# Performance work log

Hardware: AMD Instinct MI355X
Metric: run time of the kernel (lower is better)

The kernel has to match this reference:

```python
import jax, jax.numpy as jnp
import numpy as np

B, T, D = 4, 2048, 2048
P, K, ALPHA, R = 512, 16, 4, 32
E_RATIO = 0.8
EPS = 1e-6


def rmsnorm(x, g):
    return x * jax.lax.rsqrt(jnp.mean(x * x, axis=-1, keepdims=True) + EPS) * g


def dale_signs():
    # first e_ratio*P neurons excitatory (+1), rest inhibitory (-1)
    return jnp.where(jnp.arange(P) < int(E_RATIO * P), 1.0, -1.0)


def quant_dale(w, signs):
    # STE sign-quantization with per-neuron mean-abs scale + Dale's-law sign constraint
    scale = jnp.mean(jnp.abs(w), axis=-1, keepdims=True)  # [P,1]
    q = scale * signs[:, None] * jnp.ones_like(w)         # magnitude=scale, sign fixed per neuron
    return w + jax.lax.stop_gradient(q - w)


def synapse_graph(x, idx, w):
    # x: [B,T,D], idx: [P,K] int, w: [P,K] -> dendritic inputs [B,T,P,K]
    return jnp.take(x, idx, axis=-1) * w


def perceptron(x_dend, Wp, Wout, signs):
    Wq = quant_dale(Wp, signs)                              # [P,K]
    u = jnp.einsum('btpk,pk->btp', x_dend, Wq)              # [B,T,P]
    f = jax.nn.sigmoid(u)                                   # gate [B,T,P]
    f_out = quant_dale(Wout, signs)                         # [P,ALPHA]
    y = (f * u)[..., None] * f_out                          # [B,T,P,ALPHA]
    return u, f, y, f_out


def low_rank_ssm(t, f, s0, U, V, Wgate, bgate):
    # t,f: [B,T,P]; s0: [B,R]. Low-rank gated linear scan in R dims.
    z = jnp.einsum('btp,pr->btr', t, U)
    lam = jax.nn.sigmoid(jnp.einsum('btp,pr->btr', f, Wgate) + bgate)

    def step(s, inp):
        z_t, l_t = inp
        s = l_t * s + z_t
        return s, s

    sT, S = jax.lax.scan(step, s0, (jnp.moveaxis(z, 1, 0), jnp.moveaxis(lam, 1, 0)))
    tilde = jnp.einsum('btr,rp->btp', jnp.moveaxis(S, 0, 1), V)
    return tilde, sT


def flatten_ports(y):
    return y.reshape(*y.shape[:-2], P * ALPHA)


def setup_inputs() -> dict:
    key = jax.random.key(0)
    ks = jax.random.split(key, 14)
    sc = 0.1
    return {
        'x': jax.random.normal(ks[0], (B, T, D), jnp.float32),
        'state': jnp.zeros((B, R), jnp.float32),
        'g1': jnp.ones((D,), jnp.float32),
        'g2': jnp.ones((D,), jnp.float32),
        'idx_ssm': jax.random.randint(ks[1], (P, K), 0, D),
        'wg_ssm': jax.random.normal(ks[2], (P, K), jnp.float32) * sc,
        'idx_mlp': jax.random.randint(ks[3], (P, K), 0, D),
        'wg_mlp': jax.random.normal(ks[4], (P, K), jnp.float32) * sc,
        'Wp_ssm': jax.random.normal(ks[5], (P, K), jnp.float32) * sc,
        'Wout_ssm': jax.random.normal(ks[6], (P, ALPHA), jnp.float32) * sc,
        'Wp_mlp': jax.random.normal(ks[7], (P, K), jnp.float32) * sc,
        'Wout_mlp': jax.random.normal(ks[8], (P, ALPHA), jnp.float32) * sc,
        'U': jax.random.normal(ks[9], (P, R), jnp.float32) * sc,
        'V': jax.random.normal(ks[10], (R, P), jnp.float32) * sc,
        'Wgate': jax.random.normal(ks[11], (P, R), jnp.float32) * sc,
        'bgate': jnp.zeros((R,), jnp.float32),
    }


def reference(x, state, g1, g2, idx_ssm, wg_ssm, idx_mlp, wg_mlp,
              Wp_ssm, Wout_ssm, Wp_mlp, Wout_mlp, U, V, Wgate, bgate):
    signs = dale_signs()
    # --- SSM branch ---
    h1 = rmsnorm(x, g1)
    x_dend_ssm = synapse_graph(h1, idx_ssm, wg_ssm)
    u_ssm, f_ssm, _, f_out = perceptron(x_dend_ssm, Wp_ssm, Wout_ssm, signs)
    t_ssm = f_ssm * u_ssm
    tilde_t, new_state = low_rank_ssm(t_ssm, f_ssm, state, U, V, Wgate, bgate)
    y_ssm = (f_ssm * tilde_t)[..., None] * f_out            # [B,T,P,ALPHA]
    x_after = x + flatten_ports(y_ssm)
    # --- MLP branch ---
    h2 = rmsnorm(x_after, g2)
    x_dend_mlp = synapse_graph(h2, idx_mlp, wg_mlp)
    _, _, y_mlp, _ = perceptron(x_dend_mlp, Wp_mlp, Wout_mlp, signs)
    x_out = x_after + flatten_ports(y_mlp)
    return x_out, new_state
```

## Files before the change

kernel.cpp:

```cpp
#include <hip/hip_runtime.h>
#include <hip/hip_bf16.h>

#define B_ 4
#define T_ 2048
#define D_ 2048
#define P_ 512
#define K_ 16
#define ALPHA_ 4
#define R_ 32
#define NE_ 409
#define EPS_ 1e-6f
#define G_ 4

typedef unsigned short u16;

__device__ __forceinline__ float sigmoidf_(float x) {
  return 1.0f / (1.0f + __expf(-x));
}
__device__ __forceinline__ float bfb2f(u16 u) {
  return __uint_as_float(((unsigned int)u) << 16);
}
__device__ __forceinline__ u16 f2bfb(float f) {
  __hip_bfloat16 h = __float2bfloat16(f);
  return *reinterpret_cast<u16*>(&h);
}

__global__ void k_scalars(const float* __restrict__ Wp_s, const float* __restrict__ Wo_s,
                          const float* __restrict__ Wp_m, const float* __restrict__ Wo_m,
                          float* __restrict__ wq_s, float* __restrict__ fo_s,
                          float* __restrict__ wq_m, float* __restrict__ fo_m) {
  int p = blockIdx.x * blockDim.x + threadIdx.x;
  if (p >= P_) return;
  float sgn = (p < NE_) ? 1.0f : -1.0f;
  float a = 0, b = 0, c = 0, d = 0;
#pragma unroll
  for (int k = 0; k < K_; k++) {
    a += fabsf(Wp_s[p * K_ + k]);
    c += fabsf(Wp_m[p * K_ + k]);
  }
#pragma unroll
  for (int k = 0; k < ALPHA_; k++) {
    b += fabsf(Wo_s[p * ALPHA_ + k]);
    d += fabsf(Wo_m[p * ALPHA_ + k]);
  }
  wq_s[p] = sgn * a * (1.0f / K_);
  fo_s[p] = sgn * b * (1.0f / ALPHA_);
  wq_m[p] = sgn * c * (1.0f / K_);
  fo_m[p] = sgn * d * (1.0f / ALPHA_);
}

__global__ __launch_bounds__(256) void k_phase1(
    const float* __restrict__ x, const float* __restrict__ g1,
    const int* __restrict__ idx, const float* __restrict__ wg,
    const float* __restrict__ U, const float* __restrict__ Wgt,
    const float* __restrict__ bg, const float* __restrict__ wq,
    float* __restrict__ f_ssm, float* __restrict__ z, float* __restrict__ lam) {
  __shared__ u16 h1[G_][D_];
  __shared__ float fl[G_][P_];
  __shared__ float tl[G_][P_];
  __shared__ float red[G_][4];
  __shared__ float zp[G_][R_][4];
  __shared__ float lp[G_][R_][4];

  int tid = threadIdx.x;
  int token0 = blockIdx.x * G_;
  int b = token0 >> 11;
  int t0 = token0 & (T_ - 1);

  float gv[8];
  {
    const float4* gp = reinterpret_cast<const float4*>(g1 + tid * 8);
    *reinterpret_cast<float4*>(&gv[0]) = gp[0];
    *reinterpret_cast<float4*>(&gv[4]) = gp[1];
  }
  float xv[G_][8];
  float ssv[G_];
#pragma unroll
  for (int tok = 0; tok < G_; tok++) {
    const float4* xp = reinterpret_cast<const float4*>(x + (size_t)(token0 + tok) * D_ + tid * 8);
    *reinterpret_cast<float4*>(&xv[tok][0]) = xp[0];
    *reinterpret_cast<float4*>(&xv[tok][4]) = xp[1];
    float ss = 0;
#pragma unroll
    for (int i = 0; i < 8; i++) ss += xv[tok][i] * xv[tok][i];
    ssv[tok] = ss;
  }
#pragma unroll
  for (int tok = 0; tok < G_; tok++) {
    float s = ssv[tok];
#pragma unroll
    for (int off = 32; off; off >>= 1) s += __shfl_down(s, off);
    if ((tid & 63) == 0) red[tok][tid >> 6] = s;
  }
  __syncthreads();
#pragma unroll
  for (int tok = 0; tok < G_; tok++) {
    float inv = rsqrtf((red[tok][0] + red[tok][1] + red[tok][2] + red[tok][3]) * (1.0f / D_) + EPS_);
    u16 tmp[8];
#pragma unroll
    for (int i = 0; i < 8; i++) tmp[i] = f2bfb(xv[tok][i] * inv * gv[i]);
    *reinterpret_cast<uint4*>(&h1[tok][tid * 8]) = *reinterpret_cast<const uint4*>(tmp);
  }
  __syncthreads();

#pragma unroll
  for (int j = 0; j < 2; j++) {
    int p = tid + j * 256;
    union { int4 v[4]; int s[16]; } iu;
    const int4* ip = reinterpret_cast<const int4*>(idx + p * K_);
    iu.v[0] = ip[0]; iu.v[1] = ip[1]; iu.v[2] = ip[2]; iu.v[3] = ip[3];
    union { float4 v[4]; float s[16]; } wu;
    const float4* wp = reinterpret_cast<const float4*>(wg + p * K_);
    wu.v[0] = wp[0]; wu.v[1] = wp[1]; wu.v[2] = wp[2]; wu.v[3] = wp[3];
    float wqp = wq[p];
#pragma unroll
    for (int tok = 0; tok < G_; tok++) {
      float acc = 0;
#pragma unroll
      for (int k = 0; k < K_; k++) acc += bfb2f(h1[tok][iu.s[k]]) * wu.s[k];
      float u = wqp * acc;
      float f = sigmoidf_(u);
      fl[tok][p] = f;
      tl[tok][p] = f * u;
      f_ssm[(size_t)(token0 + tok) * P_ + p] = f;
    }
  }
  __syncthreads();

  int r = tid & 31, g = tid >> 5;
  float zs[G_], ls[G_];
#pragma unroll
  for (int tok = 0; tok < G_; tok++) { zs[tok] = 0; ls[tok] = 0; }
  int pbase = g * 64;
#pragma unroll 4
  for (int pp = 0; pp < 64; pp++) {
    int p = pbase + pp;
    float uu = U[p * R_ + r];
    float ww = Wgt[p * R_ + r];
#pragma unroll
    for (int tok = 0; tok < G_; tok++) {
      zs[tok] += tl[tok][p] * uu;
      ls[tok] += fl[tok][p] * ww;
    }
  }
#pragma unroll
  for (int tok = 0; tok < G_; tok++) {
    zs[tok] += __shfl_down(zs[tok], 32);
    ls[tok] += __shfl_down(ls[tok], 32);
  }
  int wid = tid >> 6;
  if ((tid & 32) == 0 && (tid & 63) < 32) {
#pragma unroll
    for (int tok = 0; tok < G_; tok++) {
      zp[tok][r][wid] = zs[tok];
      lp[tok][r][wid] = ls[tok];
    }
  }
  __syncthreads();
  if (tid < R_) {
    float bgr = bg[tid];
    float z4[G_], l4[G_];
#pragma unroll
    for (int tok = 0; tok < G_; tok++) {
      float zz = zp[tok][tid][0] + zp[tok][tid][1] + zp[tok][tid][2] + zp[tok][tid][3];
      float ll = lp[tok][tid][0] + lp[tok][tid][1] + lp[tok][tid][2] + lp[tok][tid][3];
      z4[tok] = zz;
      l4[tok] = sigmoidf_(ll + bgr);
    }
    size_t o = ((size_t)(b * R_ + tid)) * T_ + t0;
    *reinterpret_cast<float4*>(&z[o]) = *reinterpret_cast<const float4*>(z4);
    *reinterpret_cast<float4*>(&lam[o]) = *reinterpret_cast<const float4*>(l4);
  }
}

__global__ __launch_bounds__(64) void k_scan(
    const float* __restrict__ z, const float* __restrict__ lam,
    const float* __restrict__ state, float* __restrict__ S,
    float* __restrict__ out_state) {
  int br = blockIdx.x;
  int lane = threadIdx.x;
  const float* zr = z + (size_t)br * T_ + lane * 32;
  const float* lr = lam + (size_t)br * T_ + lane * 32;
  float zb[32], lb[32];
#pragma unroll
  for (int i = 0; i < 32; i += 4) {
    *reinterpret_cast<float4*>(&zb[i]) = *reinterpret_cast<const float4*>(&zr[i]);
    *reinterpret_cast<float4*>(&lb[i]) = *reinterpret_cast<const float4*>(&lr[i]);
  }
  float A = 1.0f, Z = 0.0f;
#pragma unroll
  for (int i = 0; i < 32; i++) { Z = lb[i] * Z + zb[i]; A *= lb[i]; }
  for (int off = 1; off < 64; off <<= 1) {
    float Ap = __shfl_up(A, off);
    float Zp = __shfl_up(Z, off);
    if (lane >= off) { Z = A * Zp + Z; A = A * Ap; }
  }
  float s0 = state[br];
  float Ae = __shfl_up(A, 1);
  float Ze = __shfl_up(Z, 1);
  float s = (lane == 0) ? s0 : (Ae * s0 + Ze);
  float sb[32];
#pragma unroll
  for (int i = 0; i < 32; i++) { s = lb[i] * s + zb[i]; sb[i] = s; }
  float* Sr = S + (size_t)br * T_ + lane * 32;
#pragma unroll
  for (int i = 0; i < 32; i += 4)
    *reinterpret_cast<float4*>(&Sr[i]) = *reinterpret_cast<const float4*>(&sb[i]);
  if (lane == 63) out_state[br] = s;
}

__global__ __launch_bounds__(256) void k_phase3(
    const float* __restrict__ x, const float* __restrict__ g2,
    const int* __restrict__ idx, const float* __restrict__ wg,
    const float* __restrict__ V, const float* __restrict__ S,
    const float* __restrict__ f_ssm, const float* __restrict__ fo_s,
    const float* __restrict__ wq_m, const float* __restrict__ fo_m,
    float* __restrict__ out) {
  __shared__ float Sl[G_][R_];
  __shared__ u16 h2[G_][D_];
  __shared__ float red[G_][4];

  int tid = threadIdx.x;
  int token0 = blockIdx.x * G_;
  int b = token0 >> 11;
  int t0 = token0 & (T_ - 1);

  if (tid < G_ * R_) {
    int tok = tid >> 5, r = tid & 31;
    Sl[tok][r] = S[((size_t)(b * R_ + r)) * T_ + t0 + tok];
  }
  __syncthreads();

  int p0 = 2 * tid, p1 = 2 * tid + 1;

  float til0[G_], til1[G_];
#pragma unroll
  for (int tok = 0; tok < G_; tok++) { til0[tok] = 0; til1[tok] = 0; }
#pragma unroll 4
  for (int r = 0; r < R_; r++) {
    float2 vv = *reinterpret_cast<const float2*>(V + r * P_ + p0);
#pragma unroll
    for (int tok = 0; tok < G_; tok++) {
      float s = Sl[tok][r];
      til0[tok] += s * vv.x;
      til1[tok] += s * vv.y;
    }
  }

  float2 fo = *reinterpret_cast<const float2*>(fo_s + p0);
  float gv[8];
  {
    const float4* gp = reinterpret_cast<const float4*>(g2 + tid * 8);
    *reinterpret_cast<float4*>(&gv[0]) = gp[0];
    *reinterpret_cast<float4*>(&gv[4]) = gp[1];
  }

  float xa[G_][8];
#pragma unroll
  for (int tok = 0; tok < G_; tok++) {
    float2 ff = *reinterpret_cast<const float2*>(f_ssm + (size_t)(token0 + tok) * P_ + p0);
    float val0 = ff.x * til0[tok] * fo.x;
    float val1 = ff.y * til1[tok] * fo.y;
    float xv[8];
    const float4* xp = reinterpret_cast<const float4*>(x + (size_t)(token0 + tok) * D_ + tid * 8);
    *reinterpret_cast<float4*>(&xv[0]) = xp[0];
    *reinterpret_cast<float4*>(&xv[4]) = xp[1];
    float ss = 0;
#pragma unroll
    for (int a = 0; a < 4; a++) {
      float v0 = xv[a] + val0;
      float v1 = xv[4 + a] + val1;
      xa[tok][a] = v0;
      xa[tok][4 + a] = v1;
      ss += v0 * v0 + v1 * v1;
    }
#pragma unroll
    for (int off = 32; off; off >>= 1) ss += __shfl_down(ss, off);
    if ((tid & 63) == 0) red[tok][tid >> 6] = ss;
  }
  __syncthreads();
#pragma unroll
  for (int tok = 0; tok < G_; tok++) {
    float inv = rsqrtf((red[tok][0] + red[tok][1] + red[tok][2] + red[tok][3]) * (1.0f / D_) + EPS_);
    u16 tmp[8];
#pragma unroll
    for (int i = 0; i < 8; i++) tmp[i] = f2bfb(xa[tok][i] * inv * gv[i]);
    *reinterpret_cast<uint4*>(&h2[tok][tid * 8]) = *reinterpret_cast<const uint4*>(tmp);
  }
  __syncthreads();

  union { int4 v[4]; int s[16]; } iu0, iu1;
  union { float4 v[4]; float s[16]; } wu0, wu1;
  {
    const int4* ip0 = reinterpret_cast<const int4*>(idx + p0 * K_);
    const int4* ip1 = reinterpret_cast<const int4*>(idx + p1 * K_);
    const float4* wp0 = reinterpret_cast<const float4*>(wg + p0 * K_);
    const float4* wp1 = reinterpret_cast<const float4*>(wg + p1 * K_);
#pragma unroll
    for (int q = 0; q < 4; q++) { iu0.v[q] = ip0[q]; iu1.v[q] = ip1[q]; wu0.v[q] = wp0[q]; wu1.v[q] = wp1[q]; }
  }
  float2 wqm = *reinterpret_cast<const float2*>(wq_m + p0);
  float2 fom = *reinterpret_cast<const float2*>(fo_m + p0);

#pragma unroll
  for (int tok = 0; tok < G_; tok++) {
    float acc0 = 0, acc1 = 0;
#pragma unroll
    for (int k = 0; k < K_; k++) {
      acc0 += bfb2f(h2[tok][iu0.s[k]]) * wu0.s[k];
      acc1 += bfb2f(h2[tok][iu1.s[k]]) * wu1.s[k];
    }
    float u0 = wqm.x * acc0, u1 = wqm.y * acc1;
    float f0 = sigmoidf_(u0), f1 = sigmoidf_(u1);
    float val0 = f0 * u0 * fom.x, val1 = f1 * u1 * fom.y;
    float ov[8];
#pragma unroll
    for (int a = 0; a < 4; a++) {
      ov[a] = xa[tok][a] + val0;
      ov[4 + a] = xa[tok][4 + a] + val1;
    }
    float4* op = reinterpret_cast<float4*>(out + (size_t)(token0 + tok) * D_ + tid * 8);
    op[0] = *reinterpret_cast<const float4*>(&ov[0]);
    op[1] = *reinterpret_cast<const float4*>(&ov[4]);
  }
}

extern "C" void kernel_launch(void* const* d_in, const int* in_sizes, int n_in,
                              void* d_out, int out_size, void* d_ws, size_t ws_size,
                              hipStream_t stream) {
  const float* x     = (const float*)d_in[0];
  const float* state = (const float*)d_in[1];
  const float* g1    = (const float*)d_in[2];
  const float* g2    = (const float*)d_in[3];
  const int*   idx_s = (const int*)d_in[4];
  const float* wg_s  = (const float*)d_in[5];
  const int*   idx_m = (const int*)d_in[6];
  const float* wg_m  = (const float*)d_in[7];
  const float* Wp_s  = (const float*)d_in[8];
  const float* Wo_s  = (const float*)d_in[9];
  const float* Wp_m  = (const float*)d_in[10];
  const float* Wo_m  = (const float*)d_in[11];
  const float* U     = (const float*)d_in[12];
  const float* V     = (const float*)d_in[13];
  const float* Wgt   = (const float*)d_in[14];
  const float* bg    = (const float*)d_in[15];
  float* out = (float*)d_out;

  char* ws = (char*)d_ws;
  float* wq_s = (float*)(ws + 0);
  float* fo_s = (float*)(ws + 2048);
  float* wq_m = (float*)(ws + 4096);
  float* fo_m = (float*)(ws + 6144);
  float* f_ssm = (float*)(ws + 8192);
  size_t off = 8192 + (size_t)B_ * T_ * P_ * 4;
  float* z   = (float*)(ws + off); off += (size_t)B_ * R_ * T_ * 4;
  float* lam = (float*)(ws + off); off += (size_t)B_ * R_ * T_ * 4;
  float* S   = (float*)(ws + off);

  hipLaunchKernelGGL(k_scalars, dim3(2), dim3(256), 0, stream,
                     Wp_s, Wo_s, Wp_m, Wo_m, wq_s, fo_s, wq_m, fo_m);
  hipLaunchKernelGGL(k_phase1, dim3(B_ * T_ / G_), dim3(256), 0, stream,
                     x, g1, idx_s, wg_s, U, Wgt, bg, wq_s, f_ssm, z, lam);
  hipLaunchKernelGGL(k_scan, dim3(B_ * R_), dim3(64), 0, stream,
                     z, lam, state, S, out + (size_t)B_ * T_ * D_);
  hipLaunchKernelGGL(k_phase3, dim3(B_ * T_ / G_), dim3(256), 0, stream,
                     x, g2, idx_m, wg_m, V, S, f_ssm, fo_s, wq_m, fo_m, out);
}
```

Before: 212.8 us.

## Fuse scale computation into phases, store gate activations as bf16, hoist loads

Drops the separate k_scalars launch and has each phase compute its quantization scales inline from the raw weights. The f_ssm intermediate becomes bf16 (half the global traffic), and the shared f/t buffers are packed into one u32 of two bf16s. Global loads of x, f_ssm and the index/weight rows are moved ahead of barriers to overlap latency, with launch bounds and unroll factors adjusted. This adds redundant per-block scale work and bf16 rounding on the gate values fed into the SSM.

```diff
diff --git a/kernel.cpp b/kernel.cpp
--- a/kernel.cpp
+++ b/kernel.cpp
@@ -13,51 +13,27 @@
 #define G_ 4
 
 typedef unsigned short u16;
+typedef unsigned int u32;
 
 __device__ __forceinline__ float sigmoidf_(float x) {
   return 1.0f / (1.0f + __expf(-x));
 }
-__device__ __forceinline__ float bfb2f(u16 u) {
-  return __uint_as_float(((unsigned int)u) << 16);
+__device__ __forceinline__ float bfb2f(u32 u) {
+  return __uint_as_float(u << 16);
 }
 __device__ __forceinline__ u16 f2bfb(float f) {
   __hip_bfloat16 h = __float2bfloat16(f);
   return *reinterpret_cast<u16*>(&h);
 }
 
-__global__ void k_scalars(const float* __restrict__ Wp_s, const float* __restrict__ Wo_s,
-                          const float* __restrict__ Wp_m, const float* __restrict__ Wo_m,
-                          float* __restrict__ wq_s, float* __restrict__ fo_s,
-                          float* __restrict__ wq_m, float* __restrict__ fo_m) {
-  int p = blockIdx.x * blockDim.x + threadIdx.x;
-  if (p >= P_) return;
-  float sgn = (p < NE_) ? 1.0f : -1.0f;
-  float a = 0, b = 0, c = 0, d = 0;
-#pragma unroll
-  for (int k = 0; k < K_; k++) {
-    a += fabsf(Wp_s[p * K_ + k]);
-    c += fabsf(Wp_m[p * K_ + k]);
-  }
-#pragma unroll
-  for (int k = 0; k < ALPHA_; k++) {
-    b += fabsf(Wo_s[p * ALPHA_ + k]);
-    d += fabsf(Wo_m[p * ALPHA_ + k]);
-  }
-  wq_s[p] = sgn * a * (1.0f / K_);
-  fo_s[p] = sgn * b * (1.0f / ALPHA_);
-  wq_m[p] = sgn * c * (1.0f / K_);
-  fo_m[p] = sgn * d * (1.0f / ALPHA_);
-}
-
-__global__ __launch_bounds__(256) void k_phase1(
+__global__ __launch_bounds__(256, 4) void k_phase1(
     const float* __restrict__ x, const float* __restrict__ g1,
     const int* __restrict__ idx, const float* __restrict__ wg,
     const float* __restrict__ U, const float* __restrict__ Wgt,
-    const float* __restrict__ bg, const float* __restrict__ wq,
-    float* __restrict__ f_ssm, float* __restrict__ z, float* __restrict__ lam) {
+    const float* __restrict__ bg, const float* __restrict__ Wp,
+    u16* __restrict__ f_ssm, float* __restrict__ z, float* __restrict__ lam) {
   __shared__ u16 h1[G_][D_];
-  __shared__ float fl[G_][P_];
-  __shared__ float tl[G_][P_];
+  __shared__ u32 ft[G_][P_];
   __shared__ float red[G_][4];
   __shared__ float zp[G_][R_][4];
   __shared__ float lp[G_][R_][4];
@@ -66,28 +42,41 @@
   int token0 = blockIdx.x * G_;
   int b = token0 >> 11;
   int t0 = token0 & (T_ - 1);
-
+  int p0 = 2 * tid, p1 = p0 + 1;
+
+  float xv[G_][8];
+#pragma unroll
+  for (int tok = 0; tok < G_; tok++) {
+    const float4* xp = reinterpret_cast<const float4*>(x + (size_t)(token0 + tok) * D_ + tid * 8);
+    *reinterpret_cast<float4*>(&xv[tok][0]) = xp[0];
+    *reinterpret_cast<float4*>(&xv[tok][4]) = xp[1];
+  }
   float gv[8];
   {
     const float4* gp = reinterpret_cast<const float4*>(g1 + tid * 8);
     *reinterpret_cast<float4*>(&gv[0]) = gp[0];
     *reinterpret_cast<float4*>(&gv[4]) = gp[1];
   }
-  float xv[G_][8];
-  float ssv[G_];
-#pragma unroll
-  for (int tok = 0; tok < G_; tok++) {
-    const float4* xp = reinterpret_cast<const float4*>(x + (size_t)(token0 + tok) * D_ + tid * 8);
-    *reinterpret_cast<float4*>(&xv[tok][0]) = xp[0];
-    *reinterpret_cast<float4*>(&xv[tok][4]) = xp[1];
-    float ss = 0;
-#pragma unroll
-    for (int i = 0; i < 8; i++) ss += xv[tok][i] * xv[tok][i];
-    ssv[tok] = ss;
-  }
-#pragma unroll
-  for (int tok = 0; tok < G_; tok++) {
-    float s = ssv[tok];
+  float wq0, wq1;
+  {
+    const float4* w0 = reinterpret_cast<const float4*>(Wp + p0 * K_);
+    const float4* w1 = reinterpret_cast<const float4*>(Wp + p1 * K_);
+    float a0 = 0, a1 = 0;
+#pragma unroll
+    for (int q = 0; q < 4; q++) {
+      float4 v0 = w0[q], v1 = w1[q];
+      a0 += fabsf(v0.x) + fabsf(v0.y) + fabsf(v0.z) + fabsf(v0.w);
+      a1 += fabsf(v1.x) + fabsf(v1.y) + fabsf(v1.z) + fabsf(v1.w);
+    }
+    wq0 = ((p0 < NE_) ? 1.0f : -1.0f) * a0 * (1.0f / K_);
+    wq1 = ((p1 < NE_) ? 1.0f : -1.0f) * a1 * (1.0f / K_);
+  }
+
+#pragma unroll
+  for (int tok = 0; tok < G_; tok++) {
+    float s = 0;
+#pragma unroll
+    for (int i = 0; i < 8; i++) s += xv[tok][i] * xv[tok][i];
 #pragma unroll
     for (int off = 32; off; off >>= 1) s += __shfl_down(s, off);
     if ((tid & 63) == 0) red[tok][tid >> 6] = s;
@@ -101,29 +90,34 @@
     for (int i = 0; i < 8; i++) tmp[i] = f2bfb(xv[tok][i] * inv * gv[i]);
     *reinterpret_cast<uint4*>(&h1[tok][tid * 8]) = *reinterpret_cast<const uint4*>(tmp);
   }
-  __syncthreads();
-
-#pragma unroll
-  for (int j = 0; j < 2; j++) {
-    int p = tid + j * 256;
-    union { int4 v[4]; int s[16]; } iu;
-    const int4* ip = reinterpret_cast<const int4*>(idx + p * K_);
-    iu.v[0] = ip[0]; iu.v[1] = ip[1]; iu.v[2] = ip[2]; iu.v[3] = ip[3];
-    union { float4 v[4]; float s[16]; } wu;
-    const float4* wp = reinterpret_cast<const float4*>(wg + p * K_);
-    wu.v[0] = wp[0]; wu.v[1] = wp[1]; wu.v[2] = wp[2]; wu.v[3] = wp[3];
-    float wqp = wq[p];
-#pragma unroll
-    for (int tok = 0; tok < G_; tok++) {
-      float acc = 0;
-#pragma unroll
-      for (int k = 0; k < K_; k++) acc += bfb2f(h1[tok][iu.s[k]]) * wu.s[k];
-      float u = wqp * acc;
-      float f = sigmoidf_(u);
-      fl[tok][p] = f;
-      tl[tok][p] = f * u;
-      f_ssm[(size_t)(token0 + tok) * P_ + p] = f;
-    }
+
+  union { int4 v[4]; int s[16]; } iu0, iu1;
+  union { float4 v[4]; float s[16]; } wu0, wu1;
+  {
+    const int4* ip0 = reinterpret_cast<const int4*>(idx + p0 * K_);
+    const int4* ip1 = reinterpret_cast<const int4*>(idx + p1 * K_);
+    const float4* wp0 = reinterpret_cast<const float4*>(wg + p0 * K_);
+    const float4* wp1 = reinterpret_cast<const float4*>(wg + p1 * K_);
+#pragma unroll
+    for (int q = 0; q < 4; q++) { iu0.v[q] = ip0[q]; iu1.v[q] = ip1[q]; wu0.v[q] = wp0[q]; wu1.v[q] = wp1[q]; }
+  }
+  __syncthreads();
+
+#pragma unroll
+  for (int tok = 0; tok < G_; tok++) {
+    float a0 = 0, a1 = 0;
+#pragma unroll
+    for (int k = 0; k < K_; k++) {
+      a0 += bfb2f(h1[tok][iu0.s[k]]) * wu0.s[k];
+      a1 += bfb2f(h1[tok][iu1.s[k]]) * wu1.s[k];
+    }
+    float u0 = wq0 * a0, u1 = wq1 * a1;
+    float f0 = sigmoidf_(u0), f1 = sigmoidf_(u1);
+    u32 pk0 = (u32)f2bfb(f0) | ((u32)f2bfb(f0 * u0) << 16);
+    u32 pk1 = (u32)f2bfb(f1) | ((u32)f2bfb(f1 * u1) << 16);
+    *reinterpret_cast<uint2*>(&ft[tok][p0]) = make_uint2(pk0, pk1);
+    *reinterpret_cast<u32*>(f_ssm + (size_t)(token0 + tok) * P_ + p0) =
+        (u32)f2bfb(f0) | ((u32)f2bfb(f1) << 16);
   }
   __syncthreads();
 
@@ -132,15 +126,16 @@
 #pragma unroll
   for (int tok = 0; tok < G_; tok++) { zs[tok] = 0; ls[tok] = 0; }
   int pbase = g * 64;
-#pragma unroll 4
+#pragma unroll 8
   for (int pp = 0; pp < 64; pp++) {
     int p = pbase + pp;
     float uu = U[p * R_ + r];
     float ww = Wgt[p * R_ + r];
 #pragma unroll
     for (int tok = 0; tok < G_; tok++) {
-      zs[tok] += tl[tok][p] * uu;
-      ls[tok] += fl[tok][p] * ww;
+      u32 v = ft[tok][p];
+      zs[tok] += bfb2f(v >> 16) * uu;
+      ls[tok] += bfb2f(v & 0xffffu) * ww;
     }
   }
 #pragma unroll
@@ -149,7 +144,7 @@
     ls[tok] += __shfl_down(ls[tok], 32);
   }
   int wid = tid >> 6;
-  if ((tid & 32) == 0 && (tid & 63) < 32) {
+  if ((tid & 63) < 32) {
 #pragma unroll
     for (int tok = 0; tok < G_; tok++) {
       zp[tok][r][wid] = zs[tok];
@@ -209,12 +204,12 @@
   if (lane == 63) out_state[br] = s;
 }
 
-__global__ __launch_bounds__(256) void k_phase3(
+__global__ __launch_bounds__(256, 4) void k_phase3(
     const float* __restrict__ x, const float* __restrict__ g2,
     const int* __restrict__ idx, const float* __restrict__ wg,
     const float* __restrict__ V, const float* __restrict__ S,
-    const float* __restrict__ f_ssm, const float* __restrict__ fo_s,
-    const float* __restrict__ wq_m, const float* __restrict__ fo_m,
+    const u16* __restrict__ f_ssm, const float* __restrict__ Wo_s,
+    const float* __restrict__ Wp_m, const float* __restrict__ Wo_m,
     float* __restrict__ out) {
   __shared__ float Sl[G_][R_];
   __shared__ u16 h2[G_][D_];
@@ -224,19 +219,61 @@
   int token0 = blockIdx.x * G_;
   int b = token0 >> 11;
   int t0 = token0 & (T_ - 1);
+  int p0 = 2 * tid, p1 = p0 + 1;
 
   if (tid < G_ * R_) {
     int tok = tid >> 5, r = tid & 31;
     Sl[tok][r] = S[((size_t)(b * R_ + r)) * T_ + t0 + tok];
   }
-  __syncthreads();
-
-  int p0 = 2 * tid, p1 = 2 * tid + 1;
+
+  float xa[G_][8];
+#pragma unroll
+  for (int tok = 0; tok < G_; tok++) {
+    const float4* xp = reinterpret_cast<const float4*>(x + (size_t)(token0 + tok) * D_ + tid * 8);
+    *reinterpret_cast<float4*>(&xa[tok][0]) = xp[0];
+    *reinterpret_cast<float4*>(&xa[tok][4]) = xp[1];
+  }
+  u32 fpair[G_];
+#pragma unroll
+  for (int tok = 0; tok < G_; tok++)
+    fpair[tok] = *reinterpret_cast<const u32*>(f_ssm + (size_t)(token0 + tok) * P_ + p0);
+
+  float sgn0 = (p0 < NE_) ? 1.0f : -1.0f;
+  float sgn1 = (p1 < NE_) ? 1.0f : -1.0f;
+  float fo_s0, fo_s1, fo_m0, fo_m1, wq_m0, wq_m1;
+  {
+    float4 a = *reinterpret_cast<const float4*>(Wo_s + p0 * ALPHA_);
+    float4 c = *reinterpret_cast<const float4*>(Wo_s + p1 * ALPHA_);
+    fo_s0 = sgn0 * (fabsf(a.x) + fabsf(a.y) + fabsf(a.z) + fabsf(a.w)) * (1.0f / ALPHA_);
+    fo_s1 = sgn1 * (fabsf(c.x) + fabsf(c.y) + fabsf(c.z) + fabsf(c.w)) * (1.0f / ALPHA_);
+    float4 e = *reinterpret_cast<const float4*>(Wo_m + p0 * ALPHA_);
+    float4 g = *reinterpret_cast<const float4*>(Wo_m + p1 * ALPHA_);
+    fo_m0 = sgn0 * (fabsf(e.x) + fabsf(e.y) + fabsf(e.z) + fabsf(e.w)) * (1.0f / ALPHA_);
+    fo_m1 = sgn1 * (fabsf(g.x) + fabsf(g.y) + fabsf(g.z) + fabsf(g.w)) * (1.0f / ALPHA_);
+    const float4* w0 = reinterpret_cast<const float4*>(Wp_m + p0 * K_);
+    const float4* w1 = reinterpret_cast<const float4*>(Wp_m + p1 * K_);
+    float a0 = 0, a1 = 0;
+#pragma unroll
+    for (int q = 0; q < 4; q++) {
+      float4 v0 = w0[q], v1 = w1[q];
+      a0 += fabsf(v0.x) + fabsf(v0.y) + fabsf(v0.z) + fabsf(v0.w);
+      a1 += fabsf(v1.x) + fabsf(v1.y) + fabsf(v1.z) + fabsf(v1.w);
+    }
+    wq_m0 = sgn0 * a0 * (1.0f / K_);
+    wq_m1 = sgn1 * a1 * (1.0f / K_);
+  }
+  float gv[8];
+  {
+    const float4* gp = reinterpret_cast<const float4*>(g2 + tid * 8);
+    *reinterpret_cast<float4*>(&gv[0]) = gp[0];
+    *reinterpret_cast<float4*>(&gv[4]) = gp[1];
+  }
+  __syncthreads();
 
   float til0[G_], til1[G_];
 #pragma unroll
   for (int tok = 0; tok < G_; tok++) { til0[tok] = 0; til1[tok] = 0; }
-#pragma unroll 4
+#pragma unroll 8
   for (int r = 0; r < R_; r++) {
     float2 vv = *reinterpret_cast<const float2*>(V + r * P_ + p0);
 #pragma unroll
@@ -247,32 +284,18 @@
     }
   }
 
-  float2 fo = *reinterpret_cast<const float2*>(fo_s + p0);
-  float gv[8];
-  {
-    const float4* gp = reinterpret_cast<const float4*>(g2 + tid * 8);
-    *reinterpret_cast<float4*>(&gv[0]) = gp[0];
-    *reinterpret_cast<float4*>(&gv[4]) = gp[1];
-  }
-
-  float xa[G_][8];
-#pragma unroll
-  for (int tok = 0; tok < G_; tok++) {
-    float2 ff = *reinterpret_cast<const float2*>(f_ssm + (size_t)(token0 + tok) * P_ + p0);
-    float val0 = ff.x * til0[tok] * fo.x;
-    float val1 = ff.y * til1[tok] * fo.y;
-    float xv[8];
-    const float4* xp = reinterpret_cast<const float4*>(x + (size_t)(token0 + tok) * D_ + tid * 8);
-    *reinterpret_cast<float4*>(&xv[0]) = xp[0];
-    *reinterpret_cast<float4*>(&xv[4]) = xp[1];
+#pragma unroll
+  for (int tok = 0; tok < G_; tok++) {
+    float f0 = bfb2f(fpair[tok] & 0xffffu);
+    float f1 = bfb2f(fpair[tok] >> 16);
+    float val0 = f0 * til0[tok] * fo_s0;
+    float val1 = f1 * til1[tok] * fo_s1;
     float ss = 0;
 #pragma unroll
     for (int a = 0; a < 4; a++) {
-      float v0 = xv[a] + val0;
-      float v1 = xv[4 + a] + val1;
-      xa[tok][a] = v0;
-      xa[tok][4 + a] = v1;
-      ss += v0 * v0 + v1 * v1;
+      xa[tok][a] += val0;
+      xa[tok][4 + a] += val1;
+      ss += xa[tok][a] * xa[tok][a] + xa[tok][4 + a] * xa[tok][4 + a];
     }
 #pragma unroll
     for (int off = 32; off; off >>= 1) ss += __shfl_down(ss, off);
@@ -289,39 +312,34 @@
   }
   __syncthreads();
 
-  union { int4 v[4]; int s[16]; } iu0, iu1;
-  union { float4 v[4]; float s[16]; } wu0, wu1;
-  {
-    const int4* ip0 = reinterpret_cast<const int4*>(idx + p0 * K_);
-    const int4* ip1 = reinterpret_cast<const int4*>(idx + p1 * K_);
-    const float4* wp0 = reinterpret_cast<const float4*>(wg + p0 * K_);
-    const float4* wp1 = reinterpret_cast<const float4*>(wg + p1 * K_);
-#pragma unroll
-    for (int q = 0; q < 4; q++) { iu0.v[q] = ip0[q]; iu1.v[q] = ip1[q]; wu0.v[q] = wp0[q]; wu1.v[q] = wp1[q]; }
-  }
-  float2 wqm = *reinterpret_cast<const float2*>(wq_m + p0);
-  float2 fom = *reinterpret_cast<const float2*>(fo_m + p0);
-
-#pragma unroll
-  for (int tok = 0; tok < G_; tok++) {
-    float acc0 = 0, acc1 = 0;
-#pragma unroll
-    for (int k = 0; k < K_; k++) {
-      acc0 += bfb2f(h2[tok][iu0.s[k]]) * wu0.s[k];
-      acc1 += bfb2f(h2[tok][iu1.s[k]]) * wu1.s[k];
-    }
-    float u0 = wqm.x * acc0, u1 = wqm.y * acc1;
-    float f0 = sigmoidf_(u0), f1 = sigmoidf_(u1);
-    float val0 = f0 * u0 * fom.x, val1 = f1 * u1 * fom.y;
-    float ov[8];
-#pragma unroll
-    for (int a = 0; a < 4; a++) {
-      ov[a] = xa[tok][a] + val0;
-      ov[4 + a] = xa[tok][4 + a] + val1;
-    }
+#pragma unroll
+  for (int j = 0; j < 2; j++) {
+    int p = p0 + j;
+    union { int4 v[4]; int s[16]; } iu;
+    union { float4 v[4]; float s[16]; } wu;
+    const int4* ip = reinterpret_cast<const int4*>(idx + p * K_);
+    const float4* wp = reinterpret_cast<const float4*>(wg + p * K_);
+#pragma unroll
+    for (int q = 0; q < 4; q++) { iu.v[q] = ip[q]; wu.v[q] = wp[q]; }
+    float wqm = j ? wq_m1 : wq_m0;
+    float fom = j ? fo_m1 : fo_m0;
+#pragma unroll
+    for (int tok = 0; tok < G_; tok++) {
+      float acc = 0;
+#pragma unroll
+      for (int k = 0; k < K_; k++) acc += bfb2f(h2[tok][iu.s[k]]) * wu.s[k];
+      float u = wqm * acc;
+      float f = sigmoidf_(u);
+      float val = f * u * fom;
+#pragma unroll
+      for (int a = 0; a < 4; a++) xa[tok][j * 4 + a] += val;
+    }
+  }
+#pragma unroll
+  for (int tok = 0; tok < G_; tok++) {
     float4* op = reinterpret_cast<float4*>(out + (size_t)(token0 + tok) * D_ + tid * 8);
-    op[0] = *reinterpret_cast<const float4*>(&ov[0]);
-    op[1] = *reinterpret_cast<const float4*>(&ov[4]);
+    op[0] = *reinterpret_cast<const float4*>(&xa[tok][0]);
+    op[1] = *reinterpret_cast<const float4*>(&xa[tok][4]);
   }
 }
 
@@ -347,22 +365,16 @@
   float* out = (float*)d_out;
 
   char* ws = (char*)d_ws;
-  float* wq_s = (float*)(ws + 0);
-  float* fo_s = (float*)(ws + 2048);
-  float* wq_m = (float*)(ws + 4096);
-  float* fo_m = (float*)(ws + 6144);
-  float* f_ssm = (float*)(ws + 8192);
-  size_t off = 8192 + (size_t)B_ * T_ * P_ * 4;
+  u16* f_ssm = (u16*)ws;
+  size_t off = (size_t)B_ * T_ * P_ * 2;
   float* z   = (float*)(ws + off); off += (size_t)B_ * R_ * T_ * 4;
   float* lam = (float*)(ws + off); off += (size_t)B_ * R_ * T_ * 4;
   float* S   = (float*)(ws + off);
 
-  hipLaunchKernelGGL(k_scalars, dim3(2), dim3(256), 0, stream,
-                     Wp_s, Wo_s, Wp_m, Wo_m, wq_s, fo_s, wq_m, fo_m);
   hipLaunchKernelGGL(k_phase1, dim3(B_ * T_ / G_), dim3(256), 0, stream,
-                     x, g1, idx_s, wg_s, U, Wgt, bg, wq_s, f_ssm, z, lam);
+                     x, g1, idx_s, wg_s, U, Wgt, bg, Wp_s, f_ssm, z, lam);
   hipLaunchKernelGGL(k_scan, dim3(B_ * R_), dim3(64), 0, stream,
                      z, lam, state, S, out + (size_t)B_ * T_ * D_);
   hipLaunchKernelGGL(k_phase3, dim3(B_ * T_ / G_), dim3(256), 0, stream,
-                     x, g2, idx_m, wg_m, V, S, f_ssm, fo_s, wq_m, fo_m, out);
-}
+                     x, g2, idx_m, wg_m, V, S, f_ssm, Wo_s, Wp_m, Wo_m, out);
+}
```

Measured after the change: 254.4 us. +19.5%, slower.

## Split low-rank projections into tiled kernels with packed bf16 intermediates

Applied to the files above, without the earlier changes.

Moves the U/Wgate projection out of phase1 into a separate kernel that stages U, Wgate and packed f/t values in LDS over 16-token tiles. The V projection moves into its own kernel that keeps V in LDS for 16 tokens at a time. The f and f*u gates and the tilde values are now stored as packed bf16 pairs, which halves the intermediate traffic. The scalar-precompute kernel is folded into the consumers. In exchange there are two extra launches, extra global round-trips for tilde, and bf16 rounding on values that were previously kept in fp32.

```diff
diff --git a/kernel.cpp b/kernel.cpp
--- a/kernel.cpp
+++ b/kernel.cpp
@@ -11,61 +11,31 @@
 #define NE_ 409
 #define EPS_ 1e-6f
 #define G_ 4
+#define TK_ 16
 
 typedef unsigned short u16;
+typedef unsigned int u32;
 
 __device__ __forceinline__ float sigmoidf_(float x) {
   return 1.0f / (1.0f + __expf(-x));
 }
-__device__ __forceinline__ float bfb2f(u16 u) {
-  return __uint_as_float(((unsigned int)u) << 16);
+__device__ __forceinline__ float bfb2f(u32 u) {
+  return __uint_as_float(u << 16);
 }
 __device__ __forceinline__ u16 f2bfb(float f) {
   __hip_bfloat16 h = __float2bfloat16(f);
   return *reinterpret_cast<u16*>(&h);
 }
 
-__global__ void k_scalars(const float* __restrict__ Wp_s, const float* __restrict__ Wo_s,
-                          const float* __restrict__ Wp_m, const float* __restrict__ Wo_m,
-                          float* __restrict__ wq_s, float* __restrict__ fo_s,
-                          float* __restrict__ wq_m, float* __restrict__ fo_m) {
-  int p = blockIdx.x * blockDim.x + threadIdx.x;
-  if (p >= P_) return;
-  float sgn = (p < NE_) ? 1.0f : -1.0f;
-  float a = 0, b = 0, c = 0, d = 0;
-#pragma unroll
-  for (int k = 0; k < K_; k++) {
-    a += fabsf(Wp_s[p * K_ + k]);
-    c += fabsf(Wp_m[p * K_ + k]);
-  }
-#pragma unroll
-  for (int k = 0; k < ALPHA_; k++) {
-    b += fabsf(Wo_s[p * ALPHA_ + k]);
-    d += fabsf(Wo_m[p * ALPHA_ + k]);
-  }
-  wq_s[p] = sgn * a * (1.0f / K_);
-  fo_s[p] = sgn * b * (1.0f / ALPHA_);
-  wq_m[p] = sgn * c * (1.0f / K_);
-  fo_m[p] = sgn * d * (1.0f / ALPHA_);
-}
-
-__global__ __launch_bounds__(256) void k_phase1(
+__global__ __launch_bounds__(256) void k_phase1a(
     const float* __restrict__ x, const float* __restrict__ g1,
     const int* __restrict__ idx, const float* __restrict__ wg,
-    const float* __restrict__ U, const float* __restrict__ Wgt,
-    const float* __restrict__ bg, const float* __restrict__ wq,
-    float* __restrict__ f_ssm, float* __restrict__ z, float* __restrict__ lam) {
+    const float* __restrict__ Wp, u32* __restrict__ ftg) {
   __shared__ u16 h1[G_][D_];
-  __shared__ float fl[G_][P_];
-  __shared__ float tl[G_][P_];
   __shared__ float red[G_][4];
-  __shared__ float zp[G_][R_][4];
-  __shared__ float lp[G_][R_][4];
 
   int tid = threadIdx.x;
   int token0 = blockIdx.x * G_;
-  int b = token0 >> 11;
-  int t0 = token0 & (T_ - 1);
 
   float gv[8];
   {
@@ -112,7 +82,17 @@
     union { float4 v[4]; float s[16]; } wu;
     const float4* wp = reinterpret_cast<const float4*>(wg + p * K_);
     wu.v[0] = wp[0]; wu.v[1] = wp[1]; wu.v[2] = wp[2]; wu.v[3] = wp[3];
-    float wqp = wq[p];
+    float wqp;
+    {
+      const float4* w0 = reinterpret_cast<const float4*>(Wp + p * K_);
+      float a0 = 0;
+#pragma unroll
+      for (int q = 0; q < 4; q++) {
+        float4 v0 = w0[q];
+        a0 += fabsf(v0.x) + fabsf(v0.y) + fabsf(v0.z) + fabsf(v0.w);
+      }
+      wqp = ((p < NE_) ? 1.0f : -1.0f) * a0 * (1.0f / K_);
+    }
 #pragma unroll
     for (int tok = 0; tok < G_; tok++) {
       float acc = 0;
@@ -120,57 +100,64 @@
       for (int k = 0; k < K_; k++) acc += bfb2f(h1[tok][iu.s[k]]) * wu.s[k];
       float u = wqp * acc;
       float f = sigmoidf_(u);
-      fl[tok][p] = f;
-      tl[tok][p] = f * u;
-      f_ssm[(size_t)(token0 + tok) * P_ + p] = f;
-    }
-  }
-  __syncthreads();
-
-  int r = tid & 31, g = tid >> 5;
-  float zs[G_], ls[G_];
-#pragma unroll
-  for (int tok = 0; tok < G_; tok++) { zs[tok] = 0; ls[tok] = 0; }
-  int pbase = g * 64;
-#pragma unroll 4
-  for (int pp = 0; pp < 64; pp++) {
-    int p = pbase + pp;
-    float uu = U[p * R_ + r];
-    float ww = Wgt[p * R_ + r];
-#pragma unroll
-    for (int tok = 0; tok < G_; tok++) {
-      zs[tok] += tl[tok][p] * uu;
-      ls[tok] += fl[tok][p] * ww;
-    }
-  }
-#pragma unroll
-  for (int tok = 0; tok < G_; tok++) {
-    zs[tok] += __shfl_down(zs[tok], 32);
-    ls[tok] += __shfl_down(ls[tok], 32);
-  }
-  int wid = tid >> 6;
-  if ((tid & 32) == 0 && (tid & 63) < 32) {
-#pragma unroll
-    for (int tok = 0; tok < G_; tok++) {
-      zp[tok][r][wid] = zs[tok];
-      lp[tok][r][wid] = ls[tok];
-    }
-  }
-  __syncthreads();
-  if (tid < R_) {
-    float bgr = bg[tid];
-    float z4[G_], l4[G_];
-#pragma unroll
-    for (int tok = 0; tok < G_; tok++) {
-      float zz = zp[tok][tid][0] + zp[tok][tid][1] + zp[tok][tid][2] + zp[tok][tid][3];
-      float ll = lp[tok][tid][0] + lp[tok][tid][1] + lp[tok][tid][2] + lp[tok][tid][3];
-      z4[tok] = zz;
-      l4[tok] = sigmoidf_(ll + bgr);
-    }
-    size_t o = ((size_t)(b * R_ + tid)) * T_ + t0;
-    *reinterpret_cast<float4*>(&z[o]) = *reinterpret_cast<const float4*>(z4);
-    *reinterpret_cast<float4*>(&lam[o]) = *reinterpret_cast<const float4*>(l4);
-  }
+      ftg[(size_t)(token0 + tok) * P_ + p] =
+          (u32)f2bfb(f) | ((u32)f2bfb(f * u) << 16);
+    }
+  }
+}
+
+__global__ __launch_bounds__(256) void k_zlam(
+    const u32* __restrict__ ftg, const float* __restrict__ U,
+    const float* __restrict__ Wgt, const float* __restrict__ bg,
+    float* __restrict__ z, float* __restrict__ lam) {
+  __shared__ float U_lds[128 * R_];
+  __shared__ float W_lds[128 * R_];
+  __shared__ u32 ft_lds[TK_][128];
+
+  int tid = threadIdx.x;
+  int token0 = blockIdx.x * TK_;
+  int b = token0 >> 11;
+  int tbase = token0 & (T_ - 1);
+  int r = tid & 31, tq = tid >> 5;
+
+  float z0 = 0, z1 = 0, l0 = 0, l1 = 0;
+
+  for (int c = 0; c < P_ / 128; c++) {
+    const float4* Ug = reinterpret_cast<const float4*>(U + c * 128 * R_);
+    const float4* Wg = reinterpret_cast<const float4*>(Wgt + c * 128 * R_);
+#pragma unroll
+    for (int k = 0; k < 4; k++) {
+      int vidx = k * 256 + tid;
+      reinterpret_cast<float4*>(U_lds)[vidx] = Ug[vidx];
+      reinterpret_cast<float4*>(W_lds)[vidx] = Wg[vidx];
+    }
+#pragma unroll
+    for (int k = 0; k < 2; k++) {
+      int vidx = k * 256 + tid;
+      int row = vidx >> 5, c4 = vidx & 31;
+      reinterpret_cast<uint4*>(&ft_lds[row][0])[c4] =
+          *reinterpret_cast<const uint4*>(ftg + (size_t)(token0 + row) * P_ + c * 128 + c4 * 4);
+    }
+    __syncthreads();
+#pragma unroll 8
+    for (int pp = 0; pp < 128; pp++) {
+      float uu = U_lds[pp * R_ + r];
+      float ww = W_lds[pp * R_ + r];
+      u32 v0 = ft_lds[2 * tq][pp];
+      u32 v1 = ft_lds[2 * tq + 1][pp];
+      z0 += bfb2f(v0 >> 16) * uu;
+      l0 += bfb2f(v0 & 0xffffu) * ww;
+      z1 += bfb2f(v1 >> 16) * uu;
+      l1 += bfb2f(v1 & 0xffffu) * ww;
+    }
+    __syncthreads();
+  }
+  float bgr = bg[r];
+  size_t o = ((size_t)(b * R_ + r)) * T_ + tbase + 2 * tq;
+  z[o] = z0;
+  z[o + 1] = z1;
+  lam[o] = sigmoidf_(l0 + bgr);
+  lam[o + 1] = sigmoidf_(l1 + bgr);
 }
 
 __global__ __launch_bounds__(64) void k_scan(
@@ -209,45 +196,87 @@
   if (lane == 63) out_state[br] = s;
 }
 
-__global__ __launch_bounds__(256) void k_phase3(
+__global__ __launch_bounds__(256) void k_tilde(
+    const float* __restrict__ S, const float* __restrict__ V,
+    u32* __restrict__ tilg) {
+  __shared__ float V_lds[R_ * P_];
+  __shared__ float Sl[TK_][R_];
+
+  int tid = threadIdx.x;
+  int token0 = blockIdx.x * TK_;
+  int b = token0 >> 11;
+  int tbase = token0 & (T_ - 1);
+
+#pragma unroll
+  for (int k = 0; k < 16; k++) {
+    int vidx = k * 256 + tid;
+    reinterpret_cast<float4*>(V_lds)[vidx] = reinterpret_cast<const float4*>(V)[vidx];
+  }
+#pragma unroll
+  for (int k = 0; k < 2; k++) {
+    int i = k * 256 + tid;
+    int rr = i >> 4, tok = i & 15;
+    Sl[tok][rr] = S[((size_t)(b * R_ + rr)) * T_ + tbase + tok];
+  }
+  __syncthreads();
+
+  float til0[TK_], til1[TK_];
+#pragma unroll
+  for (int tok = 0; tok < TK_; tok++) { til0[tok] = 0; til1[tok] = 0; }
+#pragma unroll 4
+  for (int rr = 0; rr < R_; rr++) {
+    float2 vv = reinterpret_cast<const float2*>(V_lds + rr * P_)[tid];
+#pragma unroll
+    for (int tok = 0; tok < TK_; tok++) {
+      float s = Sl[tok][rr];
+      til0[tok] += s * vv.x;
+      til1[tok] += s * vv.y;
+    }
+  }
+#pragma unroll
+  for (int tok = 0; tok < TK_; tok++) {
+    u32 pk = (u32)f2bfb(til0[tok]) | ((u32)f2bfb(til1[tok]) << 16);
+    tilg[((size_t)(token0 + tok) * P_ >> 1) + tid] = pk;
+  }
+}
+
+__global__ __launch_bounds__(256) void k_phase3b(
     const float* __restrict__ x, const float* __restrict__ g2,
     const int* __restrict__ idx, const float* __restrict__ wg,
-    const float* __restrict__ V, const float* __restrict__ S,
-    const float* __restrict__ f_ssm, const float* __restrict__ fo_s,
-    const float* __restrict__ wq_m, const float* __restrict__ fo_m,
-    float* __restrict__ out) {
-  __shared__ float Sl[G_][R_];
+    const u32* __restrict__ ftg, const u32* __restrict__ tilg,
+    const float* __restrict__ Wo_s, const float* __restrict__ Wp_m,
+    const float* __restrict__ Wo_m, float* __restrict__ out) {
   __shared__ u16 h2[G_][D_];
   __shared__ float red[G_][4];
 
   int tid = threadIdx.x;
   int token0 = blockIdx.x * G_;
-  int b = token0 >> 11;
-  int t0 = token0 & (T_ - 1);
-
-  if (tid < G_ * R_) {
-    int tok = tid >> 5, r = tid & 31;
-    Sl[tok][r] = S[((size_t)(b * R_ + r)) * T_ + t0 + tok];
-  }
-  __syncthreads();
-
-  int p0 = 2 * tid, p1 = 2 * tid + 1;
-
-  float til0[G_], til1[G_];
-#pragma unroll
-  for (int tok = 0; tok < G_; tok++) { til0[tok] = 0; til1[tok] = 0; }
-#pragma unroll 4
-  for (int r = 0; r < R_; r++) {
-    float2 vv = *reinterpret_cast<const float2*>(V + r * P_ + p0);
-#pragma unroll
-    for (int tok = 0; tok < G_; tok++) {
-      float s = Sl[tok][r];
-      til0[tok] += s * vv.x;
-      til1[tok] += s * vv.y;
-    }
-  }
-
-  float2 fo = *reinterpret_cast<const float2*>(fo_s + p0);
+  int p0 = 2 * tid, p1 = p0 + 1;
+
+  float sgn0 = (p0 < NE_) ? 1.0f : -1.0f;
+  float sgn1 = (p1 < NE_) ? 1.0f : -1.0f;
+  float fo_s0, fo_s1, fo_m0, fo_m1, wq_m0, wq_m1;
+  {
+    float4 a = *reinterpret_cast<const float4*>(Wo_s + p0 * ALPHA_);
+    float4 c = *reinterpret_cast<const float4*>(Wo_s + p1 * ALPHA_);
+    fo_s0 = sgn0 * (fabsf(a.x) + fabsf(a.y) + fabsf(a.z) + fabsf(a.w)) * (1.0f / ALPHA_);
+    fo_s1 = sgn1 * (fabsf(c.x) + fabsf(c.y) + fabsf(c.z) + fabsf(c.w)) * (1.0f / ALPHA_);
+    float4 e = *reinterpret_cast<const float4*>(Wo_m + p0 * ALPHA_);
+    float4 g = *reinterpret_cast<const float4*>(Wo_m + p1 * ALPHA_);
+    fo_m0 = sgn0 * (fabsf(e.x) + fabsf(e.y) + fabsf(e.z) + fabsf(e.w)) * (1.0f / ALPHA_);
+    fo_m1 = sgn1 * (fabsf(g.x) + fabsf(g.y) + fabsf(g.z) + fabsf(g.w)) * (1.0f / ALPHA_);
+    const float4* w0 = reinterpret_cast<const float4*>(Wp_m + p0 * K_);
+    const float4* w1 = reinterpret_cast<const float4*>(Wp_m + p1 * K_);
+    float a0 = 0, a1 = 0;
+#pragma unroll
+    for (int q = 0; q < 4; q++) {
+      float4 v0 = w0[q], v1 = w1[q];
+      a0 += fabsf(v0.x) + fabsf(v0.y) + fabsf(v0.z) + fabsf(v0.w);
+      a1 += fabsf(v1.x) + fabsf(v1.y) + fabsf(v1.z) + fabsf(v1.w);
+    }
+    wq_m0 = sgn0 * a0 * (1.0f / K_);
+    wq_m1 = sgn1 * a1 * (1.0f / K_);
+  }
   float gv[8];
   {
     const float4* gp = reinterpret_cast<const float4*>(g2 + tid * 8);
@@ -258,13 +287,17 @@
   float xa[G_][8];
 #pragma unroll
   for (int tok = 0; tok < G_; tok++) {
-    float2 ff = *reinterpret_cast<const float2*>(f_ssm + (size_t)(token0 + tok) * P_ + p0);
-    float val0 = ff.x * til0[tok] * fo.x;
-    float val1 = ff.y * til1[tok] * fo.y;
+    size_t trow = (size_t)(token0 + tok);
+    const float4* xp = reinterpret_cast<const float4*>(x + trow * D_ + tid * 8);
     float xv[8];
-    const float4* xp = reinterpret_cast<const float4*>(x + (size_t)(token0 + tok) * D_ + tid * 8);
     *reinterpret_cast<float4*>(&xv[0]) = xp[0];
     *reinterpret_cast<float4*>(&xv[4]) = xp[1];
+    uint2 fp = *reinterpret_cast<const uint2*>(ftg + trow * P_ + p0);
+    u32 tl = tilg[(trow * P_ >> 1) + tid];
+    float f0 = bfb2f(fp.x & 0xffffu);
+    float f1 = bfb2f(fp.y & 0xffffu);
+    float val0 = f0 * bfb2f(tl & 0xffffu) * fo_s0;
+    float val1 = f1 * bfb2f(tl >> 16) * fo_s1;
     float ss = 0;
 #pragma unroll
     for (int a = 0; a < 4; a++) {
@@ -299,8 +332,6 @@
 #pragma unroll
     for (int q = 0; q < 4; q++) { iu0.v[q] = ip0[q]; iu1.v[q] = ip1[q]; wu0.v[q] = wp0[q]; wu1.v[q] = wp1[q]; }
   }
-  float2 wqm = *reinterpret_cast<const float2*>(wq_m + p0);
-  float2 fom = *reinterpret_cast<const float2*>(fo_m + p0);
 
 #pragma unroll
   for (int tok = 0; tok < G_; tok++) {
@@ -310,9 +341,9 @@
       acc0 += bfb2f(h2[tok][iu0.s[k]]) * wu0.s[k];
       acc1 += bfb2f(h2[tok][iu1.s[k]]) * wu1.s[k];
     }
-    float u0 = wqm.x * acc0, u1 = wqm.y * acc1;
+    float u0 = wq_m0 * acc0, u1 = wq_m1 * acc1;
     float f0 = sigmoidf_(u0), f1 = sigmoidf_(u1);
-    float val0 = f0 * u0 * fom.x, val1 = f1 * u1 * fom.y;
+    float val0 = f0 * u0 * fo_m0, val1 = f1 * u1 * fo_m1;
     float ov[8];
 #pragma unroll
     for (int a = 0; a < 4; a++) {
@@ -347,22 +378,21 @@
   float* out = (float*)d_out;
 
   char* ws = (char*)d_ws;
-  float* wq_s = (float*)(ws + 0);
-  float* fo_s = (float*)(ws + 2048);
-  float* wq_m = (float*)(ws + 4096);
-  float* fo_m = (float*)(ws + 6144);
-  float* f_ssm = (float*)(ws + 8192);
-  size_t off = 8192 + (size_t)B_ * T_ * P_ * 4;
+  u32* ftg  = (u32*)ws;
+  size_t off = (size_t)B_ * T_ * P_ * 4;
   float* z   = (float*)(ws + off); off += (size_t)B_ * R_ * T_ * 4;
   float* lam = (float*)(ws + off); off += (size_t)B_ * R_ * T_ * 4;
-  float* S   = (float*)(ws + off);
-
-  hipLaunchKernelGGL(k_scalars, dim3(2), dim3(256), 0, stream,
-                     Wp_s, Wo_s, Wp_m, Wo_m, wq_s, fo_s, wq_m, fo_m);
-  hipLaunchKernelGGL(k_phase1, dim3(B_ * T_ / G_), dim3(256), 0, stream,
-                     x, g1, idx_s, wg_s, U, Wgt, bg, wq_s, f_ssm, z, lam);
+  float* S   = (float*)(ws + off); off += (size_t)B_ * R_ * T_ * 4;
+  u32* tilg  = (u32*)(ws + off);
+
+  hipLaunchKernelGGL(k_phase1a, dim3(B_ * T_ / G_), dim3(256), 0, stream,
+                     x, g1, idx_s, wg_s, Wp_s, ftg);
+  hipLaunchKernelGGL(k_zlam, dim3(B_ * T_ / TK_), dim3(256), 0, stream,
+                     ftg, U, Wgt, bg, z, lam);
   hipLaunchKernelGGL(k_scan, dim3(B_ * R_), dim3(64), 0, stream,
                      z, lam, state, S, out + (size_t)B_ * T_ * D_);
-  hipLaunchKernelGGL(k_phase3, dim3(B_ * T_ / G_), dim3(256), 0, stream,
-                     x, g2, idx_m, wg_m, V, S, f_ssm, fo_s, wq_m, fo_m, out);
-}
+  hipLaunchKernelGGL(k_tilde, dim3(B_ * T_ / TK_), dim3(256), 0, stream,
+                     S, V, tilg);
+  hipLaunchKernelGGL(k_phase3b, dim3(B_ * T_ / G_), dim3(256), 0, stream,
+                     x, g2, idx_m, wg_m, ftg, tilg, Wo_s, Wp_m, Wo_m, out);
+}
```

After: 228.7 us. +7.5%, slower.
